# Kernel tuning notes

Hardware: AMD Instinct MI355X
Metric: run time of the kernel (lower is better)

## Reference

```python
import jax, jax.numpy as jnp
import numpy as np

T_STEPS = 4
TAU = 2.0
EPS = 1e-5
NUM_HEADS = 8
SCALE = 0.125  # hardcoded self.scale in the torch module
SG_ALPHA = 4.0  # spikingjelly default sigmoid surrogate alpha


@jax.custom_vjp
def heaviside(x):
    return (x >= 0.0).astype(x.dtype)

def _hv_fwd(x):
    return heaviside(x), x

def _hv_bwd(x, g):
    s = jax.nn.sigmoid(SG_ALPHA * x)
    return (g * SG_ALPHA * s * (1.0 - s),)

heaviside.defvjp(_hv_fwd, _hv_bwd)


def lif(x_seq, v_th):
    # MultiStepLIFNode: v += (x - v)/tau; spike = H(v - v_th); hard reset to 0 (detached).
    def step(v, x):
        v = v + (x - v) / TAU
        s = heaviside(v - v_th)
        v = v * (1.0 - jax.lax.stop_gradient(s))
        return v, s
    _, out = jax.lax.scan(step, jnp.zeros_like(x_seq[0]), x_seq)
    return out


def bn(x, g, b):
    # BatchNorm1d training-mode stats over (batch, length) per channel; x: (TB, C, N)
    m = jnp.mean(x, axis=(0, 2), keepdims=True)
    var = jnp.mean((x - m) ** 2, axis=(0, 2), keepdims=True)
    return g[None, :, None] * (x - m) * jax.lax.rsqrt(var + EPS) + b[None, :, None]


def _branch(x, w, b, g, beta):
    # linear over channel dim + BN + LIF, then split heads -> (T,B,H,N,d)
    T, B, C, N = x.shape
    y = jnp.einsum('oc,tbcn->tbon', w, x) + b[None, None, :, None]
    y = bn(y.reshape(T * B, C, N), g, beta).reshape(T, B, C, N)
    y = lif(y, 1.0)
    d = C // NUM_HEADS
    return y.transpose(0, 1, 3, 2).reshape(T, B, N, NUM_HEADS, d).transpose(0, 1, 3, 2, 4)


def setup_inputs() -> dict:
    key = jax.random.key(0)
    ks = jax.random.split(key, 6)
    B, C, N = 8, 512, 1024
    bound = float(np.sqrt(6.0 / (3 * C + C)))  # xavier_uniform for (3C, C)
    return {
        'q': jax.random.normal(ks[0], (B, C, N), jnp.float32),
        'k': jax.random.normal(ks[1], (B, C, N), jnp.float32),
        'v': jax.random.normal(ks[2], (B, C, N), jnp.float32),
        'in_proj_w': jax.random.uniform(ks[3], (3 * C, C), jnp.float32, -bound, bound),
        'in_proj_b': jnp.zeros((3 * C,), jnp.float32),
        'q_gamma': jnp.ones((C,), jnp.float32),
        'q_beta': jnp.zeros((C,), jnp.float32),
        'k_gamma': jnp.ones((C,), jnp.float32),
        'k_beta': jnp.zeros((C,), jnp.float32),
        'v_gamma': jnp.ones((C,), jnp.float32),
        'v_beta': jnp.zeros((C,), jnp.float32),
        'proj_w': jax.random.normal(ks[4], (C, C), jnp.float32) * (1.0 / np.sqrt(C)),
        'proj_b': jnp.zeros((C,), jnp.float32),
        'p_gamma': jnp.ones((C,), jnp.float32),
        'p_beta': jnp.zeros((C,), jnp.float32),
    }


def reference(q, k, v, in_proj_w, in_proj_b, q_gamma, q_beta, k_gamma, k_beta,
              v_gamma, v_beta, proj_w, proj_b, p_gamma, p_beta):
    B, C, N = q.shape
    qs = jnp.broadcast_to(q[None], (T_STEPS, B, C, N))
    ks_ = jnp.broadcast_to(k[None], (T_STEPS, B, C, N))
    vs = jnp.broadcast_to(v[None], (T_STEPS, B, C, N))

    qh = _branch(qs, in_proj_w[:C], in_proj_b[:C], q_gamma, q_beta)        # (T,B,H,N,d)
    kh = _branch(ks_, in_proj_w[C:2 * C], in_proj_b[C:2 * C], k_gamma, k_beta)
    vh = _branch(vs, in_proj_w[2 * C:], in_proj_b[2 * C:], v_gamma, v_beta)

    # linear attention: (k^T v) then q @ (k^T v)
    ktv = jnp.einsum('tbhnd,tbhne->tbhde', kh, vh)            # (T,B,H,d,d)
    att = jnp.einsum('tbhnd,tbhde->tbhne', qh, ktv) * SCALE   # (T,B,H,N,d)

    x = att.transpose(0, 1, 2, 4, 3).reshape(T_STEPS, B, C, N)
    x = lif(x, 0.5)  # attn_lif with v_threshold=0.5

    z = jnp.einsum('oc,tbcn->tbon', proj_w, x) + proj_b[None, None, :, None]  # 1x1 conv
    z = bn(z.reshape(T_STEPS * B, C, N), p_gamma, p_beta).reshape(T_STEPS, B, C, N)
    return lif(z, 1.0)
```

## Files before the change

kernel.cpp:

```cpp
#include <hip/hip_runtime.h>

#define C    512
#define NDIM 1024
#define BDIM 8
#define TDIM 4
#define HDIM 8
#define CN   (C*NDIM)
#define BCN  (BDIM*CN)

typedef unsigned short u16;
typedef unsigned int   u32;
typedef unsigned long long u64;
typedef __attribute__((ext_vector_type(8))) short bf8v;
typedef __attribute__((ext_vector_type(4))) float f4v;
typedef __attribute__((ext_vector_type(2))) float f2v;

__device__ __forceinline__ u16 f2bf(float f) {
    u32 u = __float_as_uint(f);
    u32 r = u + 0x7FFFu + ((u >> 16) & 1u);
    return (u16)(r >> 16);
}
__device__ __forceinline__ float bf2f(u16 h) { return __uint_as_float((u32)h << 16); }

#if defined(__has_builtin)
#if __has_builtin(__builtin_amdgcn_global_load_lds)
#define HAS_GLL 1
#endif
#if __has_builtin(__builtin_elementwise_fma)
#define HAS_EFMA 1
#endif
#endif
#ifdef HAS_GLL
#define GLD(gp, lp) __builtin_amdgcn_global_load_lds( \
    (const __attribute__((address_space(1))) u32*)(gp), \
    (__attribute__((address_space(3))) u32*)(lp), 16, 0, 0)
#else
#define GLD(gp, lp) (*(uint4*)(lp) = *(const uint4*)(const void*)(gp))
#endif

__device__ __forceinline__ f2v pkfma(f2v a, f2v b, f2v c) {
#ifdef HAS_EFMA
    return __builtin_elementwise_fma(a, b, c);
#else
    f2v r; r.x = fmaf(a.x, b.x, c.x); r.y = fmaf(a.y, b.y, c.y); return r;
#endif
}

__global__ __launch_bounds__(256) void gemm_in3_k(
    const float* __restrict__ W, const float* __restrict__ bias,
    const float* __restrict__ Xq, const float* __restrict__ Xk,
    const float* __restrict__ Xv, float* __restrict__ Y3)
{
    __shared__ float As[16][132];
    __shared__ float Bs[16][132];
    const int tid = threadIdx.x;
    const int bz = blockIdx.z;
    const int br = bz >> 3, b = bz & 7;
    const int m0 = blockIdx.y * 128;
    const int n0 = blockIdx.x * 128;
    const float* Xb = (br == 0 ? Xq : (br == 1 ? Xk : Xv)) + (size_t)b * CN;
    const int rowOff = br * 512;

    const int ra = tid >> 2, ka = (tid & 3) * 4;
    const int kb = tid >> 5, nb = (tid & 31) * 4;
    const int tx = tid & 15, ty = tid >> 4;

    const float* pA0 = &W[(size_t)(rowOff + m0 + ra) * 512 + ka];
    const float* pA1 = &W[(size_t)(rowOff + m0 + 64 + ra) * 512 + ka];
    const float* pB0 = &Xb[(size_t)kb * NDIM + n0 + nb];
    const float* pB1 = &Xb[(size_t)(kb + 8) * NDIM + n0 + nb];

    f2v acc[2][2][4][2];
    #pragma unroll
    for (int mq = 0; mq < 2; mq++)
        #pragma unroll
        for (int nq = 0; nq < 2; nq++)
            #pragma unroll
            for (int i = 0; i < 4; i++)
                #pragma unroll
                for (int jp = 0; jp < 2; jp++) acc[mq][nq][i][jp] = (f2v){0.f, 0.f};

    float4 a0 = *(const float4*)pA0;
    float4 a1 = *(const float4*)pA1;
    float4 b0 = *(const float4*)pB0;
    float4 b1 = *(const float4*)pB1;

    for (int k0 = 0; k0 < 512; k0 += 16) {
        __syncthreads();
        As[ka + 0][ra] = a0.x; As[ka + 1][ra] = a0.y;
        As[ka + 2][ra] = a0.z; As[ka + 3][ra] = a0.w;
        As[ka + 0][64 + ra] = a1.x; As[ka + 1][64 + ra] = a1.y;
        As[ka + 2][64 + ra] = a1.z; As[ka + 3][64 + ra] = a1.w;
        *(float4*)&Bs[kb][nb]     = b0;
        *(float4*)&Bs[kb + 8][nb] = b1;
        __syncthreads();
        if (k0 < 496) {
            a0 = *(const float4*)(pA0 + k0 + 16);
            a1 = *(const float4*)(pA1 + k0 + 16);
            b0 = *(const float4*)(pB0 + (size_t)(k0 + 16) * NDIM);
            b1 = *(const float4*)(pB1 + (size_t)(k0 + 16) * NDIM);
        }
        #pragma unroll
        for (int k = 0; k < 16; k++) {
            float av[2][4];
            f2v bv[2][2];
            *(float4*)av[0] = *(const float4*)&As[k][ty * 4];
            *(float4*)av[1] = *(const float4*)&As[k][64 + ty * 4];
            float4 bq0 = *(const float4*)&Bs[k][tx * 4];
            float4 bq1 = *(const float4*)&Bs[k][64 + tx * 4];
            bv[0][0] = (f2v){bq0.x, bq0.y}; bv[0][1] = (f2v){bq0.z, bq0.w};
            bv[1][0] = (f2v){bq1.x, bq1.y}; bv[1][1] = (f2v){bq1.z, bq1.w};
            #pragma unroll
            for (int mq = 0; mq < 2; mq++)
                #pragma unroll
                for (int i = 0; i < 4; i++) {
                    const f2v a2 = (f2v){av[mq][i], av[mq][i]};
                    #pragma unroll
                    for (int nq = 0; nq < 2; nq++)
                        #pragma unroll
                        for (int jp = 0; jp < 2; jp++)
                            acc[mq][nq][i][jp] = pkfma(a2, bv[nq][jp], acc[mq][nq][i][jp]);
                }
        }
    }
    #pragma unroll
    for (int mq = 0; mq < 2; mq++)
        #pragma unroll
        for (int i = 0; i < 4; i++) {
            const int mrow = mq * 64 + ty * 4 + i;
            float bsv = bias[rowOff + m0 + mrow];
            float* yr = Y3 + (size_t)bz * CN + (size_t)(m0 + mrow) * NDIM + n0;
            #pragma unroll
            for (int nq = 0; nq < 2; nq++) {
                float4 o4 = make_float4(acc[mq][nq][i][0].x + bsv, acc[mq][nq][i][0].y + bsv,
                                        acc[mq][nq][i][1].x + bsv, acc[mq][nq][i][1].y + bsv);
                *(float4*)&yr[nq * 64 + tx * 4] = o4;
            }
        }
}

__global__ __launch_bounds__(256) void chan_stats2_k(
    const float* __restrict__ X3, float* __restrict__ mean3,
    float* __restrict__ rstd3, int outer)
{
    __shared__ float red[256];
    __shared__ float m_sh;
    const int gb = blockIdx.x;
    const int o = gb & (C - 1);
    const float* X = X3 + (size_t)(gb >> 9) * BCN;
    const int tid = threadIdx.x;
    const int total = outer * NDIM;
    float s = 0.f;
    for (int i = tid; i < total; i += 256) {
        int ou = i >> 10, n = i & 1023;
        s += X[(size_t)(ou * C + o) * NDIM + n];
    }
    red[tid] = s; __syncthreads();
    for (int off = 128; off > 0; off >>= 1) {
        if (tid < off) red[tid] += red[tid + off];
        __syncthreads();
    }
    if (tid == 0) { float m = red[0] / (float)total; mean3[gb] = m; m_sh = m; }
    __syncthreads();
    const float m = m_sh;
    float s2 = 0.f;
    for (int i = tid; i < total; i += 256) {
        int ou = i >> 10, n = i & 1023;
        float d = X[(size_t)(ou * C + o) * NDIM + n] - m;
        s2 += d * d;
    }
    red[tid] = s2; __syncthreads();
    for (int off = 128; off > 0; off >>= 1) {
        if (tid < off) red[tid] += red[tid + off];
        __syncthreads();
    }
    if (tid == 0) rstd3[gb] = 1.f / sqrtf(red[0] / (float)total + 1e-5f);
}

__global__ __launch_bounds__(256) void spikes_k(
    const float* __restrict__ Y3, const float* __restrict__ mean3,
    const float* __restrict__ rstd3,
    const float* __restrict__ qg, const float* __restrict__ qb,
    const float* __restrict__ kg, const float* __restrict__ kbt,
    const float* __restrict__ vg, const float* __restrict__ vbt,
    const float* __restrict__ PW,
    u64* __restrict__ qm, u64* __restrict__ kbits, u64* __restrict__ vbits,
    u16* __restrict__ Ps)
{
    __shared__ unsigned char tile[64][68];
    const int tid = threadIdx.x;
    const int bid = blockIdx.x;
    if (bid < 1024) {
        const int b = bid >> 7, h = (bid >> 4) & 7, nt = bid & 15;
        const int c_l = tid >> 2, sg = (tid & 3) * 16;
        const int o = h * 64 + c_l;
        const float m = mean3[o], rs = rstd3[o], g = qg[o], bt = qb[o];
        const float* Yr = Y3 + ((size_t)b * C + o) * NDIM + nt * 64 + sg;
        #pragma unroll
        for (int j = 0; j < 4; j++) {
            float4 y4 = *(const float4*)&Yr[j * 4];
            float ys[4] = {y4.x, y4.y, y4.z, y4.w};
            #pragma unroll
            for (int e = 0; e < 4; e++) {
                float x = g * (ys[e] - m);
                x = x * rs + bt;
                float v = 0.f; unsigned bits = 0;
                #pragma unroll
                for (int t = 0; t < 4; t++) {
                    v += (x - v) * 0.5f;
                    if (v - 1.0f >= 0.f) { bits |= (1u << t); v = 0.f; }
                }
                tile[c_l][sg + j * 4 + e] = (unsigned char)bits;
            }
        }
        __syncthreads();
        const int lane = tid & 63, wv = tid >> 6;
        #pragma unroll
        for (int i = 0; i < 16; i++) {
            const int nl = wv * 16 + i;
            unsigned s = tile[lane][nl];
            #pragma unroll
            for (int t = 0; t < 4; t++) {
                u64 mk = __ballot((s >> t) & 1);
                if (lane == t)
                    qm[(size_t)((t * BDIM + b) * HDIM + h) * NDIM + nt * 64 + nl] = mk;
            }
        }
    } else if (bid < 3072) {
        const int r = bid - 1024;
        const int br = r >> 10;
        const int rr = r & 1023;
        const int b = rr >> 7, ct = (rr >> 4) & 7, nt = rr & 15;
        const float* Yb = Y3 + (size_t)(br + 1) * BCN + (size_t)b * CN;
        const float* mean = mean3 + (br + 1) * C;
        const float* rstd = rstd3 + (br + 1) * C;
        const float* gam = br == 0 ? kg : vg;
        const float* bet = br == 0 ? kbt : vbt;
        u64* bits = br == 0 ? kbits : vbits;
        const int lane = tid & 63, wv = tid >> 6;
        #pragma unroll
        for (int i = 0; i < 16; i++) {
            const int o = ct * 64 + wv * 16 + i;
            const float m = mean[o], rs = rstd[o], g = gam[o], bt = bet[o];
            float y = Yb[(size_t)o * NDIM + nt * 64 + lane];
            float x = g * (y - m);
            x = x * rs + bt;
            float v = 0.f; unsigned sb = 0;
            #pragma unroll
            for (int t = 0; t < 4; t++) {
                v += (x - v) * 0.5f;
                if (v - 1.0f >= 0.f) { sb |= (1u << t); v = 0.f; }
            }
            #pragma unroll
            for (int t = 0; t < 4; t++) {
                u64 mk = __ballot((sb >> t) & 1);
                if (lane == t)
                    bits[((size_t)(t * BDIM + b) * C + o) * 16 + nt] = mk;
            }
        }
    } else {
        const int idx = (bid - 3072) * 256 + tid;
        float x = PW[idx];
        u16 h1 = f2bf(x); float r1 = x - bf2f(h1);
        u16 h2 = f2bf(r1); float r2 = r1 - bf2f(h2);
        u16 h3 = f2bf(r2);
        Ps[idx] = h1; Ps[idx + 262144] = h2; Ps[idx + 2 * 262144] = h3;
    }
}

__global__ __launch_bounds__(256) void ktv_k(
    const u64* __restrict__ kb, const u64* __restrict__ vb,
    u16* __restrict__ ktv)
{
    __shared__ u64 ks[64][17];
    __shared__ u64 vs[64][17];
    const int tid = threadIdx.x;
    const int g = blockIdx.x;
    const int h = g & 7, b = (g >> 3) & 7, t = g >> 6;
    const size_t base = ((size_t)(t * BDIM + b) * C + h * 64) * 16;
    {
        int r = tid >> 2, w0 = (tid & 3) * 4;
        #pragma unroll
        for (int j = 0; j < 4; j++) {
            ks[r][w0 + j] = kb[base + r * 16 + w0 + j];
            vs[r][w0 + j] = vb[base + r * 16 + w0 + j];
        }
    }
    __syncthreads();
    const int dd = tid >> 2, e0 = (tid & 3) * 16;
    u64 kr[16];
    #pragma unroll
    for (int w = 0; w < 16; w++) kr[w] = ks[dd][w];
    #pragma unroll
    for (int i = 0; i < 16; i++) {
        int e = e0 + i;
        int s = 0;
        #pragma unroll
        for (int w = 0; w < 16; w++) s += __popcll(kr[w] & vs[e][w]);
        ktv[(size_t)(g * 64 + dd) * 64 + e] = (u16)s;
    }
}

__global__ __launch_bounds__(256) void att_lif_k(
    const u16* __restrict__ ktv, const u64* __restrict__ qm,
    unsigned char* __restrict__ spkT)
{
    __shared__ u16 ks[4][64][64];
    const int tid = threadIdx.x;
    const int bh = blockIdx.x; const int h = bh & 7, b = bh >> 3;
    const int n0 = blockIdx.y * 64;
    #pragma unroll
    for (int t = 0; t < 4; t++) {
        const u32* src = (const u32*)&ktv[(size_t)((t * BDIM + b) * HDIM + h) * 4096];
        u32* dst = (u32*)&ks[t][0][0];
        #pragma unroll
        for (int j = 0; j < 8; j++) dst[tid + 256 * j] = src[tid + 256 * j];
    }
    __syncthreads();
    const int lane = tid & 63, wv = tid >> 6;
    for (int i = 0; i < 16; i++) {
        const int n = n0 + wv * 16 + i;
        float v = 0.f; unsigned bits = 0;
        #pragma unroll
        for (int t = 0; t < 4; t++) {
            u64 m = qm[(size_t)((t * BDIM + b) * HDIM + h) * NDIM + n];
            int acc = 0;
            while (m) {
                int dd = __ffsll(m) - 1;
                m &= m - 1;
                acc += ks[t][dd][lane];
            }
            float x = (float)acc * 0.125f;
            v += (x - v) * 0.5f;
            if (v - 0.5f >= 0.f) { bits |= (1u << t); v = 0.f; }
        }
        spkT[((size_t)b * 1024 + n) * 512 + h * 64 + lane] = (unsigned char)bits;
    }
}

__global__ __launch_bounds__(256, 2) void gemm_proj_mfma(
    const u16* __restrict__ Ps, const unsigned char* __restrict__ spkT,
    float* __restrict__ Z)
{
    __shared__ __align__(16) u16 Ab[2][12288];
    __shared__ __align__(16) u16 Bb[2][4096];
    const int tid = threadIdx.x;
    const int zb = blockIdx.z, t = zb >> 3, bb = zb & 7;
    const int m0 = blockIdx.y * 128, n0 = blockIdx.x * 128;

    u32 aoff[2][3];
    int lofs[2];
    #pragma unroll
    for (int r = 0; r < 2; r++) {
        const int cid = tid + (r << 8);
        const int mm = cid & 15, kg = (cid >> 4) & 3, mt = cid >> 6;
        lofs[r] = cid * 8;
        #pragma unroll
        for (int s = 0; s < 3; s++)
            aoff[r][s] = (u32)s * 262144u + (u32)(m0 + mt * 16 + mm) * 512u + kg * 8;
    }
    auto stageA = [&](int ki2, int p2) {
        const u32 kk = (u32)ki2 << 5;
        #pragma unroll
        for (int r = 0; r < 2; r++)
            #pragma unroll
            for (int s = 0; s < 3; s++)
                GLD(Ps + aoff[r][s] + kk, &Ab[p2][s * 4096 + lofs[r]]);
    };
    const int nn = tid & 15, ntl = (tid >> 4) & 7, seg = tid >> 7;
    const u32 srcB = ((u32)bb * 1024u + (u32)(n0 + ntl * 16 + nn)) * 512u + seg * 16;
    const int ldsB0 = (ntl * 64 + seg * 32 + nn) * 8;
    auto convB = [&](uint4 braw, int p2) {
        u32 bs[4] = {braw.x, braw.y, braw.z, braw.w};
        u32 w[8];
        #pragma unroll
        for (int qq = 0; qq < 4; qq++) {
            u32 v = bs[qq] >> t;
            w[qq * 2 + 0] = ((v & 1u) ? 0x3F80u : 0u) | ((v & 0x100u) ? 0x3F800000u : 0u);
            w[qq * 2 + 1] = (((v >> 16) & 1u) ? 0x3F80u : 0u) | ((v & 0x1000000u) ? 0x3F800000u : 0u);
        }
        *(uint4*)&Bb[p2][ldsB0]       = make_uint4(w[0], w[1], w[2], w[3]);
        *(uint4*)&Bb[p2][ldsB0 + 128] = make_uint4(w[4], w[5], w[6], w[7]);
    };

    const int lane = tid & 63, wv = tid >> 6;
    const int wm = wv >> 1, wn = wv & 1;
    const int q = lane >> 4, ln = lane & 15;
    int afo[4], bfo[4];
    #pragma unroll
    for (int i = 0; i < 4; i++) {
        afo[i] = ((wm * 4 + i) * 64 + q * 16 + ln) * 8;
        bfo[i] = ((wn * 4 + i) * 64 + q * 16 + ln) * 8;
    }

    f4v acc[4][4];
    #pragma unroll
    for (int i = 0; i < 4; i++)
        #pragma unroll
        for (int j = 0; j < 4; j++) acc[i][j] = (f4v){0.f, 0.f, 0.f, 0.f};

    stageA(0, 0);
    convB(*(const uint4*)&spkT[srcB], 0);
    uint4 braw;
    for (int ki = 0; ki < 16; ki++) {
        const int p = ki & 1;
        __syncthreads();
        if (ki < 15) {
            stageA(ki + 1, p ^ 1);
            braw = *(const uint4*)&spkT[srcB + ((u32)(ki + 1) << 5)];
        }
        bf8v bf[4];
        #pragma unroll
        for (int j = 0; j < 4; j++) bf[j] = *(const bf8v*)&Bb[p][bfo[j]];
        #pragma unroll
        for (int sa = 0; sa < 3; sa++) {
            bf8v af[4];
            #pragma unroll
            for (int i = 0; i < 4; i++) af[i] = *(const bf8v*)&Ab[p][sa * 4096 + afo[i]];
            #pragma unroll
            for (int i = 0; i < 4; i++)
                #pragma unroll
                for (int j = 0; j < 4; j++)
                    acc[i][j] = __builtin_amdgcn_mfma_f32_16x16x32_bf16(af[i], bf[j], acc[i][j], 0, 0, 0);
        }
        if (ki < 15) convB(braw, p ^ 1);
    }
    float* Zb = Z + (size_t)zb * CN;
    #pragma unroll
    for (int i = 0; i < 4; i++) {
        const int row = m0 + (wm * 4 + i) * 16 + q * 4;
        #pragma unroll
        for (int g = 0; g < 4; g++) {
            float* zr = Zb + (size_t)(row + g) * 1024 + n0 + ln;
            #pragma unroll
            for (int j = 0; j < 4; j++)
                zr[(wn * 4 + j) * 16] = acc[i][j][g];
        }
    }
}

__global__ __launch_bounds__(256) void final_bn_lif_k(
    float* __restrict__ Z, const float* __restrict__ mean,
    const float* __restrict__ rstd, const float* __restrict__ gamma,
    const float* __restrict__ beta)
{
    const int idx = blockIdx.x * 256 + threadIdx.x;
    const int o = (idx >> 10) & (C - 1);
    const float m = mean[o], rs = rstd[o], g = gamma[o], bt = beta[o];
    float v = 0.f;
    float outs[4];
    #pragma unroll
    for (int t = 0; t < 4; t++) {
        float z = Z[(size_t)t * BCN + idx];
        float x = g * (z - m);
        x = x * rs + bt;
        v += (x - v) * 0.5f;
        float s = (v - 1.0f >= 0.f) ? 1.f : 0.f;
        v *= (1.f - s);
        outs[t] = s;
    }
    #pragma unroll
    for (int t = 0; t < 4; t++) Z[(size_t)t * BCN + idx] = outs[t];
}

extern "C" void kernel_launch(void* const* d_in, const int* in_sizes, int n_in,
                              void* d_out, int out_size, void* d_ws, size_t ws_size,
                              hipStream_t stream)
{
    const float* q     = (const float*)d_in[0];
    const float* k     = (const float*)d_in[1];
    const float* v     = (const float*)d_in[2];
    const float* W     = (const float*)d_in[3];
    const float* Wb    = (const float*)d_in[4];
    const float* qg    = (const float*)d_in[5];
    const float* qb    = (const float*)d_in[6];
    const float* kg    = (const float*)d_in[7];
    const float* kbt   = (const float*)d_in[8];
    const float* vg    = (const float*)d_in[9];
    const float* vbt   = (const float*)d_in[10];
    const float* pw    = (const float*)d_in[11];
    const float* pg    = (const float*)d_in[13];
    const float* pbeta = (const float*)d_in[14];

    char* p = (char*)d_ws;
    u64* qmv = (u64*)p;                     p += (size_t)TDIM * BDIM * HDIM * NDIM * 8;
    u64* kbits = (u64*)p;                   p += (size_t)TDIM * BDIM * C * 16 * 8;
    u64* vbits = (u64*)p;                   p += (size_t)TDIM * BDIM * C * 16 * 8;
    u16* Ps = (u16*)p;                      p += (size_t)3 * 262144 * 2;
    unsigned char* spkT = (unsigned char*)p; p += (size_t)BCN;
    u16* ktv = (u16*)p;                     p += (size_t)TDIM * BDIM * HDIM * 64 * 64 * 2;
    float* mean3 = (float*)p;               p += 8192;
    float* rstd3 = (float*)p;               p += 8192;

    float* Y3 = (float*)d_out;
    float* outF = (float*)d_out;

    gemm_in3_k<<<dim3(8, 4, 24), 256, 0, stream>>>(W, Wb, q, k, v, Y3);
    chan_stats2_k<<<3 * C, 256, 0, stream>>>(Y3, mean3, rstd3, BDIM);
    spikes_k<<<4096, 256, 0, stream>>>(Y3, mean3, rstd3, qg, qb, kg, kbt, vg, vbt,
                                       pw, qmv, kbits, vbits, Ps);
    ktv_k<<<256, 256, 0, stream>>>(kbits, vbits, ktv);
    att_lif_k<<<dim3(64, 16), 256, 0, stream>>>(ktv, qmv, spkT);
    gemm_proj_mfma<<<dim3(8, 4, 32), 256, 0, stream>>>(Ps, spkT, outF);
    chan_stats2_k<<<C, 256, 0, stream>>>(outF, mean3, rstd3, TDIM * BDIM);
    final_bn_lif_k<<<BCN / 256, 256, 0, stream>>>(outF, mean3, rstd3, pg, pbeta);
}
```

Baseline: 536.8 us.

## Compute spike attention q·(kᵀv) with f16 MFMA instead of bit-scan loops

The attention kernel now expands the query spike bitmask into f16 0/1 fragments and multiplies them with a transposed f16 kᵀv matrix using 16x16x32 MFMA instructions. This replaces the per-lane loop over set bits, which gathered from LDS. The kᵀv kernel is changed to write the transposed f16 layout and no longer stages ktv through shared memory. The f16 values are exact because the counts are at most 1024, but the B fragments are now read directly from global memory.

```diff
diff --git a/kernel.cpp b/kernel.cpp
--- a/kernel.cpp
+++ b/kernel.cpp
@@ -12,6 +12,7 @@
 typedef unsigned int   u32;
 typedef unsigned long long u64;
 typedef __attribute__((ext_vector_type(8))) short bf8v;
+typedef __attribute__((ext_vector_type(8))) _Float16 h8v;
 typedef __attribute__((ext_vector_type(4))) float f4v;
 typedef __attribute__((ext_vector_type(2))) float f2v;
 
@@ -268,12 +269,12 @@
     }
 }
 
-__global__ __launch_bounds__(256) void ktv_k(
+__global__ __launch_bounds__(256) void ktvT_k(
     const u64* __restrict__ kb, const u64* __restrict__ vb,
-    u16* __restrict__ ktv)
-{
-    __shared__ u64 ks[64][17];
-    __shared__ u64 vs[64][17];
+    _Float16* __restrict__ ktvT)
+{
+    __shared__ u64 kst[64][17];
+    __shared__ u64 vst[64][17];
     const int tid = threadIdx.x;
     const int g = blockIdx.x;
     const int h = g & 7, b = (g >> 3) & 7, t = g >> 6;
@@ -282,60 +283,80 @@
         int r = tid >> 2, w0 = (tid & 3) * 4;
         #pragma unroll
         for (int j = 0; j < 4; j++) {
-            ks[r][w0 + j] = kb[base + r * 16 + w0 + j];
-            vs[r][w0 + j] = vb[base + r * 16 + w0 + j];
+            kst[r][w0 + j] = kb[base + r * 16 + w0 + j];
+            vst[r][w0 + j] = vb[base + r * 16 + w0 + j];
         }
     }
     __syncthreads();
-    const int dd = tid >> 2, e0 = (tid & 3) * 16;
-    u64 kr[16];
-    #pragma unroll
-    for (int w = 0; w < 16; w++) kr[w] = ks[dd][w];
+    const int e = tid >> 2, dd0 = (tid & 3) * 16;
+    u64 vr[16];
+    #pragma unroll
+    for (int w = 0; w < 16; w++) vr[w] = vst[e][w];
     #pragma unroll
     for (int i = 0; i < 16; i++) {
-        int e = e0 + i;
+        int dd = dd0 + i;
         int s = 0;
         #pragma unroll
-        for (int w = 0; w < 16; w++) s += __popcll(kr[w] & vs[e][w]);
-        ktv[(size_t)(g * 64 + dd) * 64 + e] = (u16)s;
-    }
-}
-
-__global__ __launch_bounds__(256) void att_lif_k(
-    const u16* __restrict__ ktv, const u64* __restrict__ qm,
+        for (int w = 0; w < 16; w++) s += __popcll(kst[dd][w] & vr[w]);
+        ktvT[(size_t)(g * 64 + e) * 64 + dd] = (_Float16)s;
+    }
+}
+
+__global__ __launch_bounds__(256) void att_mfma_k(
+    const _Float16* __restrict__ ktvT, const u64* __restrict__ qm,
     unsigned char* __restrict__ spkT)
 {
-    __shared__ u16 ks[4][64][64];
     const int tid = threadIdx.x;
+    const int w = tid >> 6, lane = tid & 63;
+    const int ln = lane & 15, q = lane >> 4;
     const int bh = blockIdx.x; const int h = bh & 7, b = bh >> 3;
-    const int n0 = blockIdx.y * 64;
+    const int n0 = blockIdx.y * 64 + w * 16;
+
+    float v[4][4];
+    u32 bits[4][4];
+    #pragma unroll
+    for (int et = 0; et < 4; et++)
+        #pragma unroll
+        for (int r = 0; r < 4; r++) { v[et][r] = 0.f; bits[et][r] = 0u; }
+
     #pragma unroll
     for (int t = 0; t < 4; t++) {
-        const u32* src = (const u32*)&ktv[(size_t)((t * BDIM + b) * HDIM + h) * 4096];
-        u32* dst = (u32*)&ks[t][0][0];
-        #pragma unroll
-        for (int j = 0; j < 8; j++) dst[tid + 256 * j] = src[tid + 256 * j];
-    }
-    __syncthreads();
-    const int lane = tid & 63, wv = tid >> 6;
-    for (int i = 0; i < 16; i++) {
-        const int n = n0 + wv * 16 + i;
-        float v = 0.f; unsigned bits = 0;
-        #pragma unroll
-        for (int t = 0; t < 4; t++) {
-            u64 m = qm[(size_t)((t * BDIM + b) * HDIM + h) * NDIM + n];
-            int acc = 0;
-            while (m) {
-                int dd = __ffsll(m) - 1;
-                m &= m - 1;
-                acc += ks[t][dd][lane];
+        const size_t gq = (size_t)(t * BDIM + b) * HDIM + h;
+        const u64 qw = qm[gq * NDIM + n0 + ln];
+        union { u16 s[8]; h8v v8; } a0u, a1u;
+        #pragma unroll
+        for (int j = 0; j < 8; j++) {
+            a0u.s[j] = (u16)(((qw >> (q * 8 + j)) & 1ull) ? 0x3C00u : 0u);
+            a1u.s[j] = (u16)(((qw >> (32 + q * 8 + j)) & 1ull) ? 0x3C00u : 0u);
+        }
+        const _Float16* kbp = ktvT + gq * 4096;
+        f4v acc[4];
+        #pragma unroll
+        for (int et = 0; et < 4; et++) acc[et] = (f4v){0.f, 0.f, 0.f, 0.f};
+        #pragma unroll
+        for (int et = 0; et < 4; et++) {
+            h8v b0 = *(const h8v*)(kbp + (et * 16 + ln) * 64 + q * 8);
+            h8v b1 = *(const h8v*)(kbp + (et * 16 + ln) * 64 + 32 + q * 8);
+            acc[et] = __builtin_amdgcn_mfma_f32_16x16x32_f16(a0u.v8, b0, acc[et], 0, 0, 0);
+            acc[et] = __builtin_amdgcn_mfma_f32_16x16x32_f16(a1u.v8, b1, acc[et], 0, 0, 0);
+        }
+        #pragma unroll
+        for (int et = 0; et < 4; et++)
+            #pragma unroll
+            for (int r = 0; r < 4; r++) {
+                float x = acc[et][r] * 0.125f;
+                float vv = v[et][r];
+                vv += (x - vv) * 0.5f;
+                if (vv - 0.5f >= 0.f) { bits[et][r] |= (1u << t); vv = 0.f; }
+                v[et][r] = vv;
             }
-            float x = (float)acc * 0.125f;
-            v += (x - v) * 0.5f;
-            if (v - 0.5f >= 0.f) { bits |= (1u << t); v = 0.f; }
-        }
-        spkT[((size_t)b * 1024 + n) * 512 + h * 64 + lane] = (unsigned char)bits;
-    }
+    }
+    #pragma unroll
+    for (int et = 0; et < 4; et++)
+        #pragma unroll
+        for (int r = 0; r < 4; r++)
+            spkT[((size_t)b * 1024 + n0 + q * 4 + r) * 512 + h * 64 + et * 16 + ln] =
+                (unsigned char)bits[et][r];
 }
 
 __global__ __launch_bounds__(256, 2) void gemm_proj_mfma(
@@ -372,15 +393,15 @@
     const int ldsB0 = (ntl * 64 + seg * 32 + nn) * 8;
     auto convB = [&](uint4 braw, int p2) {
         u32 bs[4] = {braw.x, braw.y, braw.z, braw.w};
-        u32 w[8];
+        u32 wreg[8];
         #pragma unroll
         for (int qq = 0; qq < 4; qq++) {
-            u32 v = bs[qq] >> t;
-            w[qq * 2 + 0] = ((v & 1u) ? 0x3F80u : 0u) | ((v & 0x100u) ? 0x3F800000u : 0u);
-            w[qq * 2 + 1] = (((v >> 16) & 1u) ? 0x3F80u : 0u) | ((v & 0x1000000u) ? 0x3F800000u : 0u);
-        }
-        *(uint4*)&Bb[p2][ldsB0]       = make_uint4(w[0], w[1], w[2], w[3]);
-        *(uint4*)&Bb[p2][ldsB0 + 128] = make_uint4(w[4], w[5], w[6], w[7]);
+            u32 vv = bs[qq] >> t;
+            wreg[qq * 2 + 0] = ((vv & 1u) ? 0x3F80u : 0u) | ((vv & 0x100u) ? 0x3F800000u : 0u);
+            wreg[qq * 2 + 1] = (((vv >> 16) & 1u) ? 0x3F80u : 0u) | ((vv & 0x1000000u) ? 0x3F800000u : 0u);
+        }
+        *(uint4*)&Bb[p2][ldsB0]       = make_uint4(wreg[0], wreg[1], wreg[2], wreg[3]);
+        *(uint4*)&Bb[p2][ldsB0 + 128] = make_uint4(wreg[4], wreg[5], wreg[6], wreg[7]);
     };
 
     const int lane = tid & 63, wv = tid >> 6;
@@ -488,7 +509,7 @@
     u64* vbits = (u64*)p;                   p += (size_t)TDIM * BDIM * C * 16 * 8;
     u16* Ps = (u16*)p;                      p += (size_t)3 * 262144 * 2;
     unsigned char* spkT = (unsigned char*)p; p += (size_t)BCN;
-    u16* ktv = (u16*)p;                     p += (size_t)TDIM * BDIM * HDIM * 64 * 64 * 2;
+    _Float16* ktvT = (_Float16*)p;          p += (size_t)TDIM * BDIM * HDIM * 64 * 64 * 2;
     float* mean3 = (float*)p;               p += 8192;
     float* rstd3 = (float*)p;               p += 8192;
 
@@ -499,8 +520,8 @@
     chan_stats2_k<<<3 * C, 256, 0, stream>>>(Y3, mean3, rstd3, BDIM);
     spikes_k<<<4096, 256, 0, stream>>>(Y3, mean3, rstd3, qg, qb, kg, kbt, vg, vbt,
                                        pw, qmv, kbits, vbits, Ps);
-    ktv_k<<<256, 256, 0, stream>>>(kbits, vbits, ktv);
-    att_lif_k<<<dim3(64, 16), 256, 0, stream>>>(ktv, qmv, spkT);
+    ktvT_k<<<256, 256, 0, stream>>>(kbits, vbits, ktvT);
+    att_mfma_k<<<dim3(64, 16), 256, 0, stream>>>(ktvT, qmv, spkT);
     gemm_proj_mfma<<<dim3(8, 4, 32), 256, 0, stream>>>(Ps, spkT, outF);
     chan_stats2_k<<<C, 256, 0, stream>>>(outF, mean3, rstd3, TDIM * BDIM);
     final_bn_lif_k<<<BCN / 256, 256, 0, stream>>>(outF, mean3, rstd3, pg, pbeta);
```

New measurement: 518.9 us, median of 3. 1.03x faster.
